# Performance work log

Measured on AMD Instinct MI355X. Metric: run time of the kernel, lower is better.

Reference implementation:

```python
import jax, jax.numpy as jnp
import numpy as np

N = 131072   # nodes
C = 64       # in_channels
K = 32       # n_super_nodes
B = 16       # graphs in batch
EPS = 1e-9
TAU = 1.0


def setup_inputs() -> dict:
    key = jax.random.key(0)
    ks = jax.random.split(key, 8)
    x = jax.random.normal(ks[0], (N, C), dtype=jnp.float32)
    batch = jnp.sort(jax.random.randint(ks[1], (N,), 0, B)).astype(jnp.int32)
    pos = jax.random.normal(ks[2], (N, 2), dtype=jnp.float32)
    u = jax.random.uniform(ks[3], (N, K), dtype=jnp.float32)  # uniform noise for gumbel
    W1 = jax.random.normal(ks[4], (C, C), dtype=jnp.float32) / jnp.sqrt(C)
    b1 = jnp.zeros((C,), dtype=jnp.float32)
    W2 = jax.random.normal(ks[5], (C, K), dtype=jnp.float32) / jnp.sqrt(C)
    b2 = jnp.zeros((K,), dtype=jnp.float32)
    scaling = jnp.ones((1,), dtype=jnp.float32)
    active_mask = jnp.ones((K,), dtype=jnp.float32)
    return {"x": x, "batch": batch, "pos": pos, "u": u, "W1": W1, "b1": b1,
            "W2": W2, "b2": b2, "scaling": scaling, "active_mask": active_mask}


def reference(x, batch, pos, u, W1, b1, W2, b2, scaling, active_mask):
    # assignment MLP: Linear -> ReLU -> Linear, then learned scaling
    logits = (jax.nn.relu(x @ W1 + b1) @ W2 + b2) * scaling[0]  # [N, K]
    # eval-mode masking of inactive super-nodes
    logits = jnp.where(active_mask[None, :] == 0, -1e9, logits)
    # gumbel-softmax (soft, hard=False)
    g = -jnp.log(-jnp.log(u + EPS) + EPS)
    s = jax.nn.softmax((logits + g) / TAU, axis=-1)           # [N, K]

    avg_s = s.mean(axis=0)                                     # [K]
    entropy = -jnp.mean(jnp.sum(s * jnp.log(s + EPS), axis=1))
    diversity = jnp.sum(avg_s * jnp.log(avg_s + EPS))
    pruning = jnp.mean(jnp.abs(avg_s * (1.0 - active_mask)))
    sparsity = jnp.sum(active_mask) / K

    # global spatial variance of each super-node cluster
    s_sum = s.sum(axis=0, keepdims=True) + EPS                 # [1, K]
    s_norm = s / s_sum                                         # [N, K]
    mu_g = s_norm.T @ pos                                      # [K, 2]
    pos_sq = jnp.sum(pos ** 2, axis=1, keepdims=True)          # [N, 1]
    var = (s_norm.T @ pos_sq)[:, 0] - 2.0 * jnp.sum(mu_g * (s_norm.T @ pos), axis=1) \
          + jnp.sum(mu_g ** 2, axis=1)                         # [K]
    spatial = var.mean()

    # per-graph super-node centroids via scatter-sum over batch index
    sum_s_pos = jax.ops.segment_sum(pos[:, None, :] * s[:, :, None], batch,
                                    num_segments=B)            # [B, K, 2]
    sum_s = jax.ops.segment_sum(s, batch, num_segments=B)[..., None] + EPS  # [B, K, 1]
    mu = sum_s_pos / sum_s                                     # [B, K, 2]

    # pairwise separation (repulsion) among super-node centroids
    dist_sq = jnp.sum((mu[:, :, None, :] - mu[:, None, :, :]) ** 2, axis=-1)  # [B, K, K]
    eye = jnp.eye(K, dtype=mu.dtype)[None]
    separation = jnp.sum((1.0 / (dist_sq + 1.0)) * (1.0 - eye)) / (K * (K - 1) + EPS)

    # pooled features: outer product then scatter-sum  ->  [B, K, C]
    out = jax.ops.segment_sum(x[:, None, :] * s[:, :, None], batch, num_segments=B)

    return (out, s, entropy, diversity, spatial, pruning, sparsity, separation, mu)
```

## Files before the change

kernel.cpp:

```cpp
#include <hip/hip_runtime.h>

#define EPS 1e-9f
constexpr int NN = 131072;
constexpr int CD = 64;
constexpr int KK = 32;
constexpr int BB = 16;

typedef __attribute__((ext_vector_type(8))) short short8;
typedef __attribute__((ext_vector_type(4))) float f32x4;

constexpr int WS_ENT  = 0;
constexpr int WS_BACC = 16;
constexpr int FP      = 72;
constexpr int WS_BACC_SZ = BB * KK * FP;
constexpr int WS_W1F  = WS_BACC + WS_BACC_SZ;
constexpr int WS_W2F  = WS_W1F + 2048;
constexpr int WS_B2F  = WS_W2F + 1024;
constexpr int WS_TAG  = WS_B2F + 32;
constexpr int WS_PART = 41024;
constexpr int CELLS   = 68 * 32;

constexpr int OUT_OUT  = 0;
constexpr int OUT_S    = BB * KK * CD;
constexpr int OUT_SCAL = OUT_S + NN * KK;
constexpr int OUT_MU   = OUT_SCAL + 6;

__device__ __forceinline__ unsigned short f2bf(float f) {
    unsigned b = __builtin_bit_cast(unsigned, f);
    b += 0x7fffu + ((b >> 16) & 1u);
    return (unsigned short)(b >> 16);
}

__global__ void prep_k(const float* __restrict__ W1, const float* __restrict__ W2,
                       const float* __restrict__ b2, const float* __restrict__ scaling,
                       const float* __restrict__ amask, float* __restrict__ ws) {
    const int t = threadIdx.x;
    const float sc = scaling[0];
    unsigned short* w1f = (unsigned short*)(ws + WS_W1F);
    for (int idx = t; idx < 4096; idx += 256) {
        int e = idx & 7, lane = (idx >> 3) & 63, f = idx >> 9;
        int nt = f >> 1, ks = f & 1;
        int j = nt * 16 + (lane & 15);
        int c = ks * 32 + (lane >> 4) * 8 + e;
        w1f[idx] = f2bf(W1[c * 64 + j]);
    }
    unsigned short* w2f = (unsigned short*)(ws + WS_W2F);
    for (int idx = t; idx < 2048; idx += 256) {
        int e = idx & 7, lane = (idx >> 3) & 63, f = idx >> 9;
        int nt = f >> 1, ks = f & 1;
        int j = nt * 16 + (lane & 15);
        int c = ks * 32 + (lane >> 4) * 8 + e;
        w2f[idx] = f2bf(sc * W2[c * 32 + j]);
    }
    if (t < 32) ws[WS_B2F + t] = (amask[t] == 0.f) ? -1e9f : b2[t] * sc;
}

__global__ __launch_bounds__(256)
void node_k(const float* __restrict__ x, const float* __restrict__ u,
            const float* __restrict__ b1, const float* __restrict__ ws,
            float* __restrict__ s_out, float* __restrict__ ent_acc) {
    __shared__ unsigned short Hlds[4096];
    __shared__ float Llds[64 * 33];
    __shared__ float entred[4];
    const int t = threadIdx.x;
    const int w = t >> 6, l = t & 63, lj = l & 15, lg = l >> 4;
    const unsigned short* w1f = (const unsigned short*)(ws + WS_W1F);
    const unsigned short* w2f = (const unsigned short*)(ws + WS_W2F);
    const float* b2f = ws + WS_B2F;

    const int node = blockIdx.x * 64 + w * 16 + lj;
    const float* xr = x + (size_t)node * 64 + lg * 8;
    short8 a0, a1;
    {
        float4 p0 = *(const float4*)xr;
        float4 p1 = *(const float4*)(xr + 4);
        float4 p2 = *(const float4*)(xr + 32);
        float4 p3 = *(const float4*)(xr + 36);
        a0[0] = f2bf(p0.x); a0[1] = f2bf(p0.y); a0[2] = f2bf(p0.z); a0[3] = f2bf(p0.w);
        a0[4] = f2bf(p1.x); a0[5] = f2bf(p1.y); a0[6] = f2bf(p1.z); a0[7] = f2bf(p1.w);
        a1[0] = f2bf(p2.x); a1[1] = f2bf(p2.y); a1[2] = f2bf(p2.z); a1[3] = f2bf(p2.w);
        a1[4] = f2bf(p3.x); a1[5] = f2bf(p3.y); a1[6] = f2bf(p3.z); a1[7] = f2bf(p3.w);
    }
    f32x4 hacc[4];
#pragma unroll
    for (int nt = 0; nt < 4; nt++) {
        f32x4 acc = {0.f, 0.f, 0.f, 0.f};
        short8 b0 = *(const short8*)(w1f + (nt * 2 + 0) * 512 + l * 8);
        short8 b1v = *(const short8*)(w1f + (nt * 2 + 1) * 512 + l * 8);
        acc = __builtin_amdgcn_mfma_f32_16x16x32_bf16(a0, b0, acc, 0, 0, 0);
        acc = __builtin_amdgcn_mfma_f32_16x16x32_bf16(a1, b1v, acc, 0, 0, 0);
        hacc[nt] = acc;
    }
#pragma unroll
    for (int nt = 0; nt < 4; nt++) {
        const float bias = b1[nt * 16 + lj];
#pragma unroll
        for (int q = 0; q < 4; q++) {
            const int r = lg * 4 + q;
            const float hv = fmaxf(hacc[nt][q] + bias, 0.f);
            const int bo = (nt * 32 + lj * 2) ^ ((r & 7) << 4);
            Hlds[w * 1024 + r * 64 + (bo >> 1)] = f2bf(hv);
        }
    }
    short8 a20, a21;
    {
        const int base = w * 1024 + lj * 64;
        a20 = *(const short8*)(Hlds + base + ((lg ^ (lj & 7)) << 3));
        a21 = *(const short8*)(Hlds + base + (((4 + lg) ^ (lj & 7)) << 3));
    }
#pragma unroll
    for (int nt = 0; nt < 2; nt++) {
        f32x4 acc = {0.f, 0.f, 0.f, 0.f};
        short8 b0 = *(const short8*)(w2f + (nt * 2 + 0) * 512 + l * 8);
        short8 b1v = *(const short8*)(w2f + (nt * 2 + 1) * 512 + l * 8);
        acc = __builtin_amdgcn_mfma_f32_16x16x32_bf16(a20, b0, acc, 0, 0, 0);
        acc = __builtin_amdgcn_mfma_f32_16x16x32_bf16(a21, b1v, acc, 0, 0, 0);
        const float bb = b2f[nt * 16 + lj];
#pragma unroll
        for (int q = 0; q < 4; q++)
            Llds[(w * 16 + lg * 4 + q) * 33 + nt * 16 + lj] = acc[q] + bb;
    }
    __syncthreads();

    const int nl = t >> 2, sub = t & 3;
    const int n = blockIdx.x * 64 + nl;
    const float* Lr = &Llds[nl * 33 + sub * 8];
    const float* ur = u + (size_t)n * 32 + sub * 8;
    float4 u0 = *(const float4*)ur, u1 = *(const float4*)(ur + 4);
    float uu[8] = {u0.x, u0.y, u0.z, u0.w, u1.x, u1.y, u1.z, u1.w};
    float z[8];
    float m = -3.0e38f;
#pragma unroll
    for (int i = 0; i < 8; i++) {
        float g = -__logf(-__logf(uu[i] + EPS) + EPS);
        z[i] = Lr[i] + g;
        m = fmaxf(m, z[i]);
    }
    m = fmaxf(m, __shfl_xor(m, 1, 64));
    m = fmaxf(m, __shfl_xor(m, 2, 64));
    float es = 0.f;
#pragma unroll
    for (int i = 0; i < 8; i++) { z[i] = __expf(z[i] - m); es += z[i]; }
    es += __shfl_xor(es, 1, 64);
    es += __shfl_xor(es, 2, 64);
    const float inv = 1.f / es;
    float ent = 0.f;
#pragma unroll
    for (int i = 0; i < 8; i++) {
        float sv = z[i] * inv;
        z[i] = sv;
        ent += sv * __logf(sv + EPS);
    }
    float* so = s_out + (size_t)n * 32 + sub * 8;
    *(float4*)so = make_float4(z[0], z[1], z[2], z[3]);
    *(float4*)(so + 4) = make_float4(z[4], z[5], z[6], z[7]);
#pragma unroll
    for (int off = 32; off > 0; off >>= 1) ent += __shfl_down(ent, off, 64);
    if (l == 0) entred[w] = ent;
    __syncthreads();
    if (t == 0) atomicAdd(ent_acc, entred[0] + entred[1] + entred[2] + entred[3]);
}

__global__ void pool_k(const float* __restrict__ s,
                       const float* __restrict__ x,
                       const float* __restrict__ pos,
                       const int* __restrict__ batch,
                       float* __restrict__ bacc,
                       float* __restrict__ part,
                       int* __restrict__ tags,
                       int npb) {
    const int t = threadIdx.x;
    const int k = t & 31;
    const int fg = t >> 5;
    const int base = blockIdx.x * npb;
    float acc[8];
    float accx = 0.f;
#pragma unroll
    for (int f = 0; f < 8; f++) acc[f] = 0.f;
    int cur_b = batch[base];
#pragma unroll 2
    for (int n = base; n < base + npb; n++) {
        const int b = batch[n];
        if (b != cur_b) {
            float* dst = bacc + (cur_b * 32 + k) * FP;
#pragma unroll
            for (int f = 0; f < 8; f++) { atomicAdd(dst + fg * 8 + f, acc[f]); acc[f] = 0.f; }
            if (fg < 4) { atomicAdd(dst + 64 + fg, accx); accx = 0.f; }
            cur_b = b;
        }
        const float sv = s[n * 32 + k];
        const float4 v0 = *(const float4*)(x + n * 64 + fg * 8);
        const float4 v1 = *(const float4*)(x + n * 64 + fg * 8 + 4);
        acc[0] = fmaf(sv, v0.x, acc[0]);
        acc[1] = fmaf(sv, v0.y, acc[1]);
        acc[2] = fmaf(sv, v0.z, acc[2]);
        acc[3] = fmaf(sv, v0.w, acc[3]);
        acc[4] = fmaf(sv, v1.x, acc[4]);
        acc[5] = fmaf(sv, v1.y, acc[5]);
        acc[6] = fmaf(sv, v1.z, acc[6]);
        acc[7] = fmaf(sv, v1.w, acc[7]);
        if (fg < 4) {
            float2 p = *(const float2*)(pos + n * 2);
            float e = (fg == 0) ? p.x : (fg == 1) ? p.y
                    : (fg == 2) ? (p.x * p.x + p.y * p.y) : 1.f;
            accx = fmaf(sv, e, accx);
        }
    }
    float* pp = part + (size_t)blockIdx.x * CELLS;
#pragma unroll
    for (int f = 0; f < 8; f++) pp[(fg * 8 + f) * 32 + k] = acc[f];
    if (fg < 4) pp[(64 + fg) * 32 + k] = accx;
    if (t == 0) tags[blockIdx.x] = cur_b;
}

__global__ void reduce_k(const float* __restrict__ part,
                         const int* __restrict__ tags,
                         float* __restrict__ bacc,
                         float* __restrict__ outp,
                         int nblk) {
    const int b = blockIdx.x;
    const int cell = blockIdx.y * 256 + threadIdx.x;
    if (cell >= CELLS) return;
    const int k = cell & 31, f = cell >> 5;
    int lo = 0, hi = nblk;
    while (lo < hi) { int mid = (lo + hi) >> 1; if (tags[mid] < b) lo = mid + 1; else hi = mid; }
    int lo2 = lo, hi2 = nblk;
    while (lo2 < hi2) { int mid = (lo2 + hi2) >> 1; if (tags[mid] < b + 1) lo2 = mid + 1; else hi2 = mid; }
    float v = 0.f;
    for (int blk = lo; blk < lo2; blk++)
        v += part[(size_t)blk * CELLS + cell];
    const int idx = (b * 32 + k) * FP + f;
    const float tot = bacc[idx] + v;
    bacc[idx] = tot;
    if (f < 64) outp[OUT_OUT + ((b * 32 + k) << 6) + f] = tot;
}

__global__ void fin_k(const float* __restrict__ ws,
                      const float* __restrict__ amask,
                      float* __restrict__ outp) {
    const int t = threadIdx.x;
    const float* bacc = ws + WS_BACC;
    __shared__ float mu_s[BB * KK * 2];
    for (int idx = t; idx < BB * KK * 2; idx += 256) {
        int bk = idx >> 1, d = idx & 1;
        float v = bacc[bk * FP + 64 + d] / (bacc[bk * FP + 67] + EPS);
        mu_s[idx] = v;
        outp[OUT_MU + idx] = v;
    }
    __shared__ float kred[32][4];
    if (t < 32) {
        float S = 0, px = 0, py = 0, sq = 0;
        for (int b = 0; b < 16; b++) {
            const float* pp = bacc + (b * 32 + t) * FP;
            S += pp[67]; px += pp[64]; py += pp[65]; sq += pp[66];
        }
        float avg = S / (float)NN;
        float am = amask[t];
        float ssum = S + EPS;
        float mx = px / ssum, my = py / ssum;
        kred[t][0] = avg * __logf(avg + EPS);
        kred[t][1] = fabsf(avg * (1.f - am));
        kred[t][2] = sq / ssum - mx * mx - my * my;
        kred[t][3] = am;
    }
    __syncthreads();
    float sep = 0.f;
    for (int idx = t; idx < BB * KK * KK; idx += 256) {
        int b = idx >> 10, i = (idx >> 5) & 31, j = idx & 31;
        if (i != j) {
            float dx = mu_s[(b * 32 + i) * 2 + 0] - mu_s[(b * 32 + j) * 2 + 0];
            float dy = mu_s[(b * 32 + i) * 2 + 1] - mu_s[(b * 32 + j) * 2 + 1];
            sep += 1.f / (dx * dx + dy * dy + 1.f);
        }
    }
    __shared__ float red[256];
    red[t] = sep;
    __syncthreads();
    for (int s2 = 128; s2 > 0; s2 >>= 1) {
        if (t < s2) red[t] += red[t + s2];
        __syncthreads();
    }
    if (t == 0) {
        float div = 0, pru = 0, spa = 0, spar = 0;
        for (int kq = 0; kq < 32; kq++) {
            div += kred[kq][0]; pru += kred[kq][1];
            spa += kred[kq][2]; spar += kred[kq][3];
        }
        outp[OUT_SCAL + 0] = -ws[WS_ENT] / (float)NN;
        outp[OUT_SCAL + 1] = div;
        outp[OUT_SCAL + 2] = spa / 32.f;
        outp[OUT_SCAL + 3] = pru / 32.f;
        outp[OUT_SCAL + 4] = spar / 32.f;
        outp[OUT_SCAL + 5] = red[0] / (32.f * 31.f + EPS);
    }
}

extern "C" void kernel_launch(void* const* d_in, const int* in_sizes, int n_in,
                              void* d_out, int out_size, void* d_ws, size_t ws_size,
                              hipStream_t stream) {
    const float* x       = (const float*)d_in[0];
    const int*   batch   = (const int*)d_in[1];
    const float* pos     = (const float*)d_in[2];
    const float* u       = (const float*)d_in[3];
    const float* W1      = (const float*)d_in[4];
    const float* b1      = (const float*)d_in[5];
    const float* W2      = (const float*)d_in[6];
    const float* b2      = (const float*)d_in[7];
    const float* scaling = (const float*)d_in[8];
    const float* amask   = (const float*)d_in[9];
    float* outp = (float*)d_out;
    float* ws   = (float*)d_ws;

    int npb = 128;
    while (npb < NN &&
           ws_size < ((size_t)WS_PART + (size_t)(NN / npb) * CELLS) * sizeof(float))
        npb <<= 1;
    const int nblk = NN / npb;

    hipMemsetAsync(ws, 0, (size_t)(WS_BACC + WS_BACC_SZ) * sizeof(float), stream);
    prep_k<<<1, 256, 0, stream>>>(W1, W2, b2, scaling, amask, ws);
    node_k<<<NN / 64, 256, 0, stream>>>(x, u, b1, ws, outp + OUT_S, ws + WS_ENT);
    pool_k<<<nblk, 256, 0, stream>>>(outp + OUT_S, x, pos, batch,
                                     ws + WS_BACC, ws + WS_PART, (int*)(ws + WS_TAG), npb);
    reduce_k<<<dim3(BB, (CELLS + 255) / 256), 256, 0, stream>>>(
        ws + WS_PART, (const int*)(ws + WS_TAG), ws + WS_BACC, outp, nblk);
    fin_k<<<1, 256, 0, stream>>>(ws, amask, outp);
}
```

Measured before the change: 220.0 us.

## Restructure pool kernel to per-wave node ranges with lane-per-feature accumulators

The pooling kernel now splits each block's node range across its four waves. Each lane owns one feature channel and keeps 32 super-node accumulators, reading x once per node coalesced and taking s values as broadcast reads. This removes the redundant s reads and the per-thread float4 loads of the old 8-features-per-thread layout. Per-wave partials are merged through LDS atomics and written in a k-major, 68-wide layout, and reduce_k's cell indexing is changed to match. The cost is more registers and the extra LDS atomics for the merge.

After: 224.2 us. Within noise of the previous version (+1.9%).

```diff
diff --git a/kernel.cpp b/kernel.cpp
--- a/kernel.cpp
+++ b/kernel.cpp
@@ -161,56 +161,77 @@
     if (t == 0) atomicAdd(ent_acc, entred[0] + entred[1] + entred[2] + entred[3]);
 }
 
-__global__ void pool_k(const float* __restrict__ s,
-                       const float* __restrict__ x,
-                       const float* __restrict__ pos,
-                       const int* __restrict__ batch,
-                       float* __restrict__ bacc,
-                       float* __restrict__ part,
-                       int* __restrict__ tags,
-                       int npb) {
+__global__ __launch_bounds__(256)
+void pool_k(const float* __restrict__ s, const float* __restrict__ x,
+            const float* __restrict__ pos, const int* __restrict__ batch,
+            float* __restrict__ bacc, float* __restrict__ part,
+            int* __restrict__ tags, int npb) {
+    __shared__ float Plds[CELLS];
     const int t = threadIdx.x;
-    const int k = t & 31;
-    const int fg = t >> 5;
+    const int l = t & 63;
+    const int w = __builtin_amdgcn_readfirstlane(t >> 6);
+    for (int idx = t; idx < CELLS; idx += 256) Plds[idx] = 0.f;
     const int base = blockIdx.x * npb;
-    float acc[8];
-    float accx = 0.f;
-#pragma unroll
-    for (int f = 0; f < 8; f++) acc[f] = 0.f;
-    int cur_b = batch[base];
+    const int wn = npb >> 2;
+    const int n0 = base + w * wn, n1 = n0 + wn;
+    float acc[32];
+#pragma unroll
+    for (int kk = 0; kk < 32; kk++) acc[kk] = 0.f;
+    float a2x = 0.f, a2y = 0.f, a2q = 0.f, a2s = 0.f;
+    int cur_b = batch[n0];
+    __syncthreads();
 #pragma unroll 2
-    for (int n = base; n < base + npb; n++) {
+    for (int n = n0; n < n1; n++) {
         const int b = batch[n];
         if (b != cur_b) {
-            float* dst = bacc + (cur_b * 32 + k) * FP;
-#pragma unroll
-            for (int f = 0; f < 8; f++) { atomicAdd(dst + fg * 8 + f, acc[f]); acc[f] = 0.f; }
-            if (fg < 4) { atomicAdd(dst + 64 + fg, accx); accx = 0.f; }
+            float* dst = bacc + (cur_b * 32) * FP + l;
+#pragma unroll
+            for (int kk = 0; kk < 32; kk++) { atomicAdd(dst + kk * FP, acc[kk]); acc[kk] = 0.f; }
+            if (l < 32) {
+                float* d2 = bacc + (cur_b * 32 + l) * FP + 64;
+                atomicAdd(d2 + 0, a2x); atomicAdd(d2 + 1, a2y);
+                atomicAdd(d2 + 2, a2q); atomicAdd(d2 + 3, a2s);
+                a2x = a2y = a2q = a2s = 0.f;
+            }
             cur_b = b;
         }
-        const float sv = s[n * 32 + k];
-        const float4 v0 = *(const float4*)(x + n * 64 + fg * 8);
-        const float4 v1 = *(const float4*)(x + n * 64 + fg * 8 + 4);
-        acc[0] = fmaf(sv, v0.x, acc[0]);
-        acc[1] = fmaf(sv, v0.y, acc[1]);
-        acc[2] = fmaf(sv, v0.z, acc[2]);
-        acc[3] = fmaf(sv, v0.w, acc[3]);
-        acc[4] = fmaf(sv, v1.x, acc[4]);
-        acc[5] = fmaf(sv, v1.y, acc[5]);
-        acc[6] = fmaf(sv, v1.z, acc[6]);
-        acc[7] = fmaf(sv, v1.w, acc[7]);
-        if (fg < 4) {
-            float2 p = *(const float2*)(pos + n * 2);
-            float e = (fg == 0) ? p.x : (fg == 1) ? p.y
-                    : (fg == 2) ? (p.x * p.x + p.y * p.y) : 1.f;
-            accx = fmaf(sv, e, accx);
-        }
-    }
+        const float xv = x[(size_t)n * 64 + l];
+        const float sv = s[(size_t)n * 32 + (l & 31)];
+        const float* sr = s + (size_t)n * 32;
+#pragma unroll
+        for (int kk = 0; kk < 32; kk++)
+            acc[kk] = fmaf(sr[kk], xv, acc[kk]);
+        const float* pr = pos + (size_t)n * 2;
+        const float px = pr[0], py = pr[1];
+        const float tx = sv * px, ty = sv * py;
+        a2x += tx; a2y += ty;
+        a2q = fmaf(tx, px, fmaf(ty, py, a2q));
+        a2s += sv;
+    }
+    const int tagb = batch[base + npb - 1];
+    if (cur_b == tagb) {
+#pragma unroll
+        for (int kk = 0; kk < 32; kk++) atomicAdd(&Plds[kk * 68 + l], acc[kk]);
+        if (l < 32) {
+            atomicAdd(&Plds[l * 68 + 64], a2x);
+            atomicAdd(&Plds[l * 68 + 65], a2y);
+            atomicAdd(&Plds[l * 68 + 66], a2q);
+            atomicAdd(&Plds[l * 68 + 67], a2s);
+        }
+    } else {
+        float* dst = bacc + (cur_b * 32) * FP + l;
+#pragma unroll
+        for (int kk = 0; kk < 32; kk++) atomicAdd(dst + kk * FP, acc[kk]);
+        if (l < 32) {
+            float* d2 = bacc + (cur_b * 32 + l) * FP + 64;
+            atomicAdd(d2 + 0, a2x); atomicAdd(d2 + 1, a2y);
+            atomicAdd(d2 + 2, a2q); atomicAdd(d2 + 3, a2s);
+        }
+    }
+    __syncthreads();
     float* pp = part + (size_t)blockIdx.x * CELLS;
-#pragma unroll
-    for (int f = 0; f < 8; f++) pp[(fg * 8 + f) * 32 + k] = acc[f];
-    if (fg < 4) pp[(64 + fg) * 32 + k] = accx;
-    if (t == 0) tags[blockIdx.x] = cur_b;
+    for (int idx = t; idx < CELLS; idx += 256) pp[idx] = Plds[idx];
+    if (t == 0) tags[blockIdx.x] = tagb;
 }
 
 __global__ void reduce_k(const float* __restrict__ part,
@@ -221,12 +242,13 @@
     const int b = blockIdx.x;
     const int cell = blockIdx.y * 256 + threadIdx.x;
     if (cell >= CELLS) return;
-    const int k = cell & 31, f = cell >> 5;
+    const int k = cell / 68, f = cell - k * 68;
     int lo = 0, hi = nblk;
     while (lo < hi) { int mid = (lo + hi) >> 1; if (tags[mid] < b) lo = mid + 1; else hi = mid; }
     int lo2 = lo, hi2 = nblk;
     while (lo2 < hi2) { int mid = (lo2 + hi2) >> 1; if (tags[mid] < b + 1) lo2 = mid + 1; else hi2 = mid; }
     float v = 0.f;
+#pragma unroll 4
     for (int blk = lo; blk < lo2; blk++)
         v += part[(size_t)blk * CELLS + cell];
     const int idx = (b * 32 + k) * FP + f;
```
